# Kernel optimization log

Measured on AMD Instinct MI355X. Metric: run time of the kernel, lower is better.

Reference implementation:

```python
import jax, jax.numpy as jnp
import numpy as np

BSZ = 64
SEQ = 64      # logits rows per sequence (cu_seqlens_q stride)
CAND = 32     # candidates per batch == block_size
VOCAB = 32000
TOTAL = BSZ * CAND


def setup_inputs() -> dict:
    key = jax.random.key(0)
    k1, k2, k3, k4, k5 = jax.random.split(key, 5)
    input_logits = jax.random.normal(k1, (BSZ * SEQ, VOCAB), dtype=jnp.float32)
    relative_idx = jax.random.randint(k2, (TOTAL,), 0, SEQ, dtype=jnp.int32)
    batch_offsets = jnp.arange(BSZ, dtype=jnp.int32) * SEQ
    cu_filtered = jnp.arange(BSZ + 1, dtype=jnp.int32) * CAND
    cu_seqlens_q = jnp.arange(BSZ + 1, dtype=jnp.int32) * SEQ
    temperatures = 0.5 + 1.5 * jax.random.uniform(k3, (TOTAL,), dtype=jnp.float32)
    num_transfer = jax.random.randint(k4, (BSZ,), 0, 16, dtype=jnp.int32)
    thresholds = 0.3 * jax.random.uniform(k5, (BSZ,), dtype=jnp.float32)
    top_p = jnp.full((1,), 0.9, dtype=jnp.float32)
    return {
        'input_logits': input_logits, 'relative_idx': relative_idx,
        'batch_offsets': batch_offsets, 'cu_filtered': cu_filtered,
        'cu_seqlens_q': cu_seqlens_q, 'temperatures': temperatures,
        'num_transfer': num_transfer, 'thresholds': thresholds,
        'top_p': top_p, 'top_k': 50, 'block_size': CAND,
    }


def reference(input_logits, relative_idx, batch_offsets, cu_filtered, cu_seqlens_q,
              temperatures, num_transfer, thresholds, top_p, top_k, block_size):
    bsz = cu_filtered.shape[0] - 1
    total = relative_idx.shape[0]
    vocab = input_logits.shape[-1]
    NEG = jnp.finfo(input_logits.dtype).min

    # triton_repeat_interleave: group id of each candidate token
    counts = cu_filtered[1:] - cu_filtered[:-1]                      # [B]
    group_ids = jnp.repeat(jnp.arange(bsz), counts, total_repeat_length=total)
    k_values = jnp.maximum(num_transfer, 0)

    # gather candidate logits rows
    global_rows = cu_seqlens_q[:-1][group_ids] + relative_idx        # [T]
    cand = jnp.take(input_logits, global_rows, axis=0)               # [T, V]
    scaled = cand / temperatures[:, None]

    # top_k_logits
    kk = min(int(top_k), vocab)
    topk_vals = jax.lax.top_k(scaled, kk)[0]                         # [T, kk]
    thr_k = topk_vals[:, kk - 1][:, None]
    scaled = jnp.where(scaled < thr_k, NEG, scaled)

    # top_p_logits (nucleus)
    order = jnp.argsort(-scaled, axis=-1)                            # descending
    sorted_logits = jnp.take_along_axis(scaled, order, axis=-1)
    cum = jnp.cumsum(jax.nn.softmax(sorted_logits, axis=-1), axis=-1)
    remove = cum > top_p.reshape(-1, 1)
    remove = jnp.concatenate([jnp.zeros_like(remove[:, :1]), remove[:, :-1]], axis=-1)
    inv = jnp.argsort(order, axis=-1)                                # inverse permutation
    mask = jnp.take_along_axis(remove, inv, axis=-1)
    scaled = jnp.where(mask, NEG, scaled)

    probs = jax.nn.softmax(scaled, axis=-1)
    top_probs = probs.max(axis=-1)                                   # scores ('confidence')
    top_tokens = probs.argmax(axis=-1).astype(jnp.int32)             # greedy sample_token
    abs_idx = relative_idx + batch_offsets[group_ids]

    # ragged_to_dense: [B, block_size], padded with -inf / 0 / 0
    pos_in_row = jnp.arange(block_size)[None, :]                     # [1, L]
    row_mask = pos_in_row < counts[:, None]                          # [B, L]
    flat = jnp.where(row_mask, cu_filtered[:-1, None] + pos_in_row, 0)
    dense_scores = jnp.where(row_mask, top_probs[flat], -jnp.inf)
    dense_tokens = jnp.where(row_mask, top_tokens[flat], 0)
    dense_pos = jnp.where(row_mask, abs_idx[flat], 0)

    # per-row descending sort by score (padding -inf sorts last)
    sort_idx = jnp.argsort(-dense_scores, axis=1)
    sorted_scores = jnp.take_along_axis(dense_scores, sort_idx, axis=1)
    sorted_tokens = jnp.take_along_axis(dense_tokens, sort_idx, axis=1)
    sorted_pos = jnp.take_along_axis(dense_pos, sort_idx, axis=1)

    # filter_and_count
    keep = (pos_in_row < k_values[:, None]) \
        & (sorted_scores >= thresholds[:, None]) \
        & (sorted_scores > -jnp.inf)
    out_tokens = jnp.where(keep, sorted_tokens, -1)
    out_pos = jnp.where(keep, sorted_pos, 0)
    out_counts = keep.sum(axis=1).astype(jnp.int32)
    return out_pos, out_tokens, out_counts
```

## Files before the change

kernel.cpp:

```cpp
#include <hip/hip_runtime.h>
#include <math.h>

#define THREADS 256
#define CAP 512
#define HIST_BINS 4096
#define RAW_THRESH 2.5f

typedef float f32x4 __attribute__((ext_vector_type(4)));

__device__ __forceinline__ unsigned orderKey(float f) {
    unsigned u = __float_as_uint(f);
    return (u & 0x80000000u) ? ~u : (u | 0x80000000u);
}

struct WS {
    float* svals; int* sidx; int* wsn;
    float* prob; int* tok;
};
__device__ __forceinline__ WS ws_layout(void* ws, int nrows, int total) {
    WS w;
    w.svals = (float*)ws;
    w.sidx  = (int*)(w.svals + (size_t)nrows * CAP);
    w.wsn   = w.sidx + (size_t)nrows * CAP;
    w.prob  = (float*)(w.wsn + nrows);
    w.tok   = (int*)(w.prob + total);
    return w;
}

#define COLLECT1(x, gi) \
    if ((x) >= RAW_THRESH) { int p = atomicAdd(&s_n, 1); if (p < CAP) { u.a.v[p] = (x); u.a.id[p] = (gi); } }
#define COLLECT4(vv, base) \
    COLLECT1((vv).x, (base)) COLLECT1((vv).y, (base) + 1) \
    COLLECT1((vv).z, (base) + 2) COLLECT1((vv).w, (base) + 3)

__global__ __launch_bounds__(THREADS, 8) void row_kernel(
    const float* __restrict__ logits,
    const int* __restrict__ rel_idx,
    const int* __restrict__ cuf,
    const int* __restrict__ cuq,
    const int* __restrict__ topk_p,
    int bsz, int total, long long logits_n, void* ws)
{
    __shared__ union {
        struct { float v[CAP]; int id[CAP]; float sv[CAP]; int si[CAP]; } a;
        int hist[HIST_BINS];
    } u;
    __shared__ int s_n, s_needed;
    __shared__ unsigned s_T, s_maxkey;

    const int tid = threadIdx.x;
    const int nrows = cuq[bsz];
    const int vocab = (int)(logits_n / (long long)nrows);
    int kk = topk_p[0];
    if (kk > vocab) kk = vocab;

    WS w = ws_layout(ws, nrows, total);

    for (int r = blockIdx.x; r < nrows; r += gridDim.x) {
        int lo = 0, hi = bsz;
        while (hi - lo > 1) { int mid = (lo + hi) >> 1; if (r >= cuq[mid]) lo = mid; else hi = mid; }
        const int b = lo;
        const int rel = r - cuq[b];

        if (tid == 0) { s_needed = 0; s_n = 0; }
        __syncthreads();
        const int t0 = cuf[b], cnt = cuf[b + 1] - t0;
        for (int l = tid; l < cnt; l += THREADS)
            if (rel_idx[t0 + l] == rel) s_needed = 1;
        __syncthreads();
        if (!s_needed) continue;

        const float* rp = logits + (long long)r * (long long)vocab;
        const f32x4* rp4 = (const f32x4*)rp;
        const int nv4 = vocab >> 2;

        int i = tid;
        for (; i + THREADS < nv4; i += 2 * THREADS) {
            f32x4 a = rp4[i];
            f32x4 c = rp4[i + THREADS];
            float mx = fmaxf(fmaxf(fmaxf(a.x, a.y), fmaxf(a.z, a.w)),
                             fmaxf(fmaxf(c.x, c.y), fmaxf(c.z, c.w)));
            if (mx >= RAW_THRESH) {
                COLLECT4(a, i << 2)
                COLLECT4(c, (i + THREADS) << 2)
            }
        }
        for (; i < nv4; i += THREADS) {
            f32x4 a = rp4[i];
            float mx = fmaxf(fmaxf(a.x, a.y), fmaxf(a.z, a.w));
            if (mx >= RAW_THRESH) {
                COLLECT4(a, i << 2)
            }
        }
        for (int j = (nv4 << 2) + tid; j < vocab; j += THREADS) {
            float x = rp[j];
            COLLECT1(x, j)
        }
        __syncthreads();
        int n = s_n;

        if (n < kk || n > CAP) {
            __syncthreads();
            for (int j = tid; j < HIST_BINS; j += THREADS) u.hist[j] = 0;
            if (tid == 0) { s_n = 0; s_maxkey = 0; }
            __syncthreads();
            for (int j = tid; j < vocab; j += THREADS) {
                unsigned k = orderKey(rp[j]);
                atomicAdd(&u.hist[k >> 20], 1);
                atomicMax(&s_maxkey, k);
            }
            __syncthreads();
            if (tid == 0) {
                int B = (int)(s_maxkey >> 20);
                int cum = 0;
                while (true) {
                    cum += u.hist[B];
                    if (cum >= kk || B == 0) break;
                    --B;
                }
                s_T = ((unsigned)B) << 20;
            }
            __syncthreads();
            const unsigned Tk = s_T;
            __syncthreads();
            for (int j = tid; j < vocab; j += THREADS) {
                float a = rp[j];
                if (orderKey(a) >= Tk) {
                    int p = atomicAdd(&s_n, 1);
                    if (p < CAP) { u.a.v[p] = a; u.a.id[p] = j; }
                }
            }
            __syncthreads();
            n = s_n;
            if (n > CAP) n = CAP;
        }

        for (int j = tid; j < n; j += THREADS) {
            float v = u.a.v[j];
            int id = u.a.id[j];
            int rk = 0;
            for (int q = 0; q < n; ++q) {
                float x = u.a.v[q];
                rk += (x > v) || (x == v && u.a.id[q] < id);
            }
            u.a.sv[rk] = v;
            u.a.si[rk] = id;
        }
        __syncthreads();
        for (int j = tid; j < n; j += THREADS) {
            w.svals[(size_t)r * CAP + j] = u.a.sv[j];
            w.sidx[(size_t)r * CAP + j]  = u.a.si[j];
        }
        if (tid == 0) w.wsn[r] = n;
        __syncthreads();
    }
}

__global__ __launch_bounds__(64) void token_kernel(
    const float* __restrict__ logits,
    const int* __restrict__ rel_idx,
    const int* __restrict__ cuf,
    const int* __restrict__ cuq,
    const float* __restrict__ temps,
    const int* __restrict__ topk_p,
    const float* __restrict__ topp_p,
    int bsz, int total, long long logits_n, void* ws)
{
    __shared__ union {
        struct { float sv[CAP]; int si[CAP]; float e[CAP]; } a;
        int hist[HIST_BINS];
    } u;
    __shared__ int s_m, s_amax, s_n;
    __shared__ unsigned s_T, s_maxkey;

    const int t = blockIdx.x;
    const int l = threadIdx.x;
    const int nrows = cuq[bsz];
    const int vocab = (int)(logits_n / (long long)nrows);
    int kk = topk_p[0];
    if (kk > vocab) kk = vocab;

    WS w = ws_layout(ws, nrows, total);

    int lo = 0, hi = bsz;
    while (hi - lo > 1) { int mid = (lo + hi) >> 1; if (t >= cuf[mid]) lo = mid; else hi = mid; }
    const int row = cuq[lo] + rel_idx[t];
    const float T = temps[t];
    const float* rp = logits + (long long)row * (long long)vocab;
    int n = w.wsn[row];

    if (n >= kk && n <= CAP) {
        for (int j = l; j < n; j += 64) {
            u.a.sv[j] = w.svals[(size_t)row * CAP + j] / T;
            u.a.si[j] = w.sidx[(size_t)row * CAP + j];
        }
        __syncthreads();
    } else {
        for (int j = l; j < HIST_BINS; j += 64) u.hist[j] = 0;
        if (l == 0) { s_n = 0; s_maxkey = 0; }
        __syncthreads();
        for (int j = l; j < vocab; j += 64) {
            unsigned k = orderKey(rp[j]);
            atomicAdd(&u.hist[k >> 20], 1);
            atomicMax(&s_maxkey, k);
        }
        __syncthreads();
        if (l == 0) {
            int B = (int)(s_maxkey >> 20);
            int cum = 0;
            while (true) {
                cum += u.hist[B];
                if (cum >= kk || B == 0) break;
                --B;
            }
            s_T = ((unsigned)B) << 20;
        }
        __syncthreads();
        const unsigned Tk = s_T;
        __syncthreads();
        for (int j = l; j < vocab; j += 64) {
            float a = rp[j];
            if (orderKey(a) >= Tk) {
                int p = atomicAdd(&s_n, 1);
                if (p < CAP) { u.a.sv[p] = a / T; u.a.si[p] = j; }
            }
        }
        __syncthreads();
        n = s_n;
        if (n > CAP) n = CAP;
        if (kk > n) kk = n;
        float v = 0.f; int id = 0; int rk = -1;
        for (int j = l; j < n; j += 64) {
            v = u.a.sv[j]; id = u.a.si[j];
            int r2 = 0;
            for (int q = 0; q < n; ++q) {
                float x = u.a.sv[q];
                r2 += (x > v) || (x == v && u.a.si[q] < id);
            }
            rk = r2;
            break;
        }
        float vs[CAP / 64]; int ids[CAP / 64]; int rks[CAP / 64]; int cnt2 = 0;
        for (int j = l; j < n; j += 64) {
            float vv = u.a.sv[j]; int ii = u.a.si[j];
            int r2 = 0;
            for (int q = 0; q < n; ++q) {
                float x = u.a.sv[q];
                r2 += (x > vv) || (x == vv && u.a.si[q] < ii);
            }
            vs[cnt2] = vv; ids[cnt2] = ii; rks[cnt2] = r2; ++cnt2;
        }
        __syncthreads();
        for (int j2 = 0; j2 < cnt2; ++j2) { u.a.sv[rks[j2]] = vs[j2]; u.a.si[rks[j2]] = ids[j2]; }
        __syncthreads();
        (void)v; (void)id; (void)rk;
    }

    const float M = u.a.sv[0];
    const float thrk = u.a.sv[kk - 1];

    int mcnt = 0;
    int cand = 0x7fffffff;
    for (int j = l; j < n; j += 64) {
        mcnt += (u.a.sv[j] >= thrk) ? 1 : 0;
        if (u.a.sv[j] == M && u.a.si[j] < cand) cand = u.a.si[j];
    }
    for (int off = 32; off > 0; off >>= 1) {
        mcnt += __shfl_down(mcnt, off);
        int oc = __shfl_down(cand, off);
        if (oc < cand) cand = oc;
    }
    if (l == 0) { s_m = mcnt; s_amax = cand; }
    __syncthreads();
    const int m = s_m;
    for (int j = l; j < m; j += 64) u.a.e[j] = expf(u.a.sv[j] - M);
    __syncthreads();
    if (l == 0) {
        float Z1 = 0.f;
        for (int j = 0; j < m; ++j) Z1 += u.a.e[j];
        const float topp = topp_p[0];
        int jcut = m - 1;
        float c = 0.f;
        for (int j = 0; j < m; ++j) {
            float p = u.a.e[j] / Z1;
            c += p;
            if (c > topp) { jcut = j; break; }
        }
        float Z2 = 0.f;
        for (int j = 0; j <= jcut; ++j) Z2 += u.a.e[j];
        w.prob[t] = 1.0f / Z2;
        w.tok[t] = s_amax;
    }
}

__global__ __launch_bounds__(64) void finalize_kernel(
    const int* __restrict__ rel_idx,
    const int* __restrict__ boff,
    const int* __restrict__ cuf,
    const int* __restrict__ cuq,
    const int* __restrict__ num_transfer,
    const float* __restrict__ thresholds,
    int bsz, int total, int L,
    void* ws,
    int* __restrict__ out)
{
    const int bq = blockIdx.x;
    const int l = threadIdx.x;
    const int nrows = cuq[bsz];
    WS w = ws_layout(ws, nrows, total);

    const int start = cuf[bq];
    int cnt = cuf[bq + 1] - start;
    if (cnt > L) cnt = L;

    __shared__ float ss[64]; __shared__ int stk[64]; __shared__ int sp[64];
    __shared__ float ss2[64]; __shared__ int stk2[64]; __shared__ int sp2[64];

    float score = -INFINITY; int tk = 0; int pos = 0;
    if (l < L) {
        if (l < cnt) {
            int t = start + l;
            score = w.prob[t];
            tk = w.tok[t];
            pos = rel_idx[t] + boff[bq];
        }
        ss[l] = score; stk[l] = tk; sp[l] = pos;
    }
    __syncthreads();
    if (l < L) {
        int r = 0;
        for (int j = 0; j < L; ++j) {
            float x = ss[j];
            r += (x > score) || (x == score && j < l);
        }
        ss2[r] = score; stk2[r] = tk; sp2[r] = pos;
    }
    __syncthreads();

    int k = num_transfer[bq]; if (k < 0) k = 0;
    const float thrb = thresholds[bq];
    bool kp = false;
    if (l < L) {
        float s = ss2[l];
        kp = (l < k) && (s >= thrb) && (s > -INFINITY);
        out[bq * L + l] = kp ? sp2[l] : 0;
        out[bsz * L + bq * L + l] = kp ? stk2[l] : -1;
    }
    unsigned long long mask = __ballot(kp);
    if (l == 0) out[2 * bsz * L + bq] = (int)__popcll(mask);
}

extern "C" void kernel_launch(void* const* d_in, const int* in_sizes, int n_in,
                              void* d_out, int out_size, void* d_ws, size_t ws_size,
                              hipStream_t stream) {
    const float* logits   = (const float*)d_in[0];
    const int*   rel      = (const int*)d_in[1];
    const int*   boff     = (const int*)d_in[2];
    const int*   cuf      = (const int*)d_in[3];
    const int*   cuq      = (const int*)d_in[4];
    const float* temps    = (const float*)d_in[5];
    const int*   ntr      = (const int*)d_in[6];
    const float* thr      = (const float*)d_in[7];
    const float* topp     = (const float*)d_in[8];
    const int*   topk     = (const int*)d_in[9];

    const int total = in_sizes[1];
    const int bsz   = in_sizes[6];
    const long long logits_n = (long long)in_sizes[0];
    const int L = (out_size - bsz) / (2 * bsz);

    row_kernel<<<2 * total, THREADS, 0, stream>>>(
        logits, rel, cuf, cuq, topk, bsz, total, logits_n, d_ws);

    token_kernel<<<total, 64, 0, stream>>>(
        logits, rel, cuf, cuq, temps, topk, topp, bsz, total, logits_n, d_ws);

    finalize_kernel<<<bsz, 64, 0, stream>>>(
        rel, boff, cuf, cuq, ntr, thr, bsz, total, L, d_ws, (int*)d_out);
}
```

Before: 80.73 us.

## Precompute needed-row list and distribute rows via atomic work queue

```diff
diff --git a/kernel.cpp b/kernel.cpp
--- a/kernel.cpp
+++ b/kernel.cpp
@@ -14,12 +14,18 @@
 }
 
 struct WS {
+    int* mark;
+    int* rowlist;
+    int* meta;
     float* svals; int* sidx; int* wsn;
     float* prob; int* tok;
 };
 __device__ __forceinline__ WS ws_layout(void* ws, int nrows, int total) {
     WS w;
-    w.svals = (float*)ws;
+    w.mark = (int*)ws;
+    w.rowlist = w.mark + nrows;
+    w.meta = w.rowlist + nrows;
+    w.svals = (float*)(w.meta + 8);
     w.sidx  = (int*)(w.svals + (size_t)nrows * CAP);
     w.wsn   = w.sidx + (size_t)nrows * CAP;
     w.prob  = (float*)(w.wsn + nrows);
@@ -27,6 +33,31 @@
     return w;
 }
 
+__global__ void zero_kernel(const int* __restrict__ cuq, int bsz, int total, void* ws) {
+    const int nrows = cuq[bsz];
+    WS w = ws_layout(ws, nrows, total);
+    for (int i = blockIdx.x * blockDim.x + threadIdx.x; i < nrows; i += gridDim.x * blockDim.x)
+        w.mark[i] = 0;
+    if (blockIdx.x == 0 && threadIdx.x < 8) w.meta[threadIdx.x] = 0;
+}
+
+__global__ void mark_kernel(const int* __restrict__ rel_idx,
+                            const int* __restrict__ cuf,
+                            const int* __restrict__ cuq,
+                            int bsz, int total, void* ws) {
+    const int t = blockIdx.x * blockDim.x + threadIdx.x;
+    if (t >= total) return;
+    const int nrows = cuq[bsz];
+    WS w = ws_layout(ws, nrows, total);
+    int lo = 0, hi = bsz;
+    while (hi - lo > 1) { int mid = (lo + hi) >> 1; if (t >= cuf[mid]) lo = mid; else hi = mid; }
+    const int row = cuq[lo] + rel_idx[t];
+    if (atomicCAS(&w.mark[row], 0, 1) == 0) {
+        int p = atomicAdd(&w.meta[0], 1);
+        w.rowlist[p] = row;
+    }
+}
+
 #define COLLECT1(x, gi) \
     if ((x) >= RAW_THRESH) { int p = atomicAdd(&s_n, 1); if (p < CAP) { u.a.v[p] = (x); u.a.id[p] = (gi); } }
 #define COLLECT4(vv, base) \
@@ -35,8 +66,6 @@
 
 __global__ __launch_bounds__(THREADS, 8) void row_kernel(
     const float* __restrict__ logits,
-    const int* __restrict__ rel_idx,
-    const int* __restrict__ cuf,
     const int* __restrict__ cuq,
     const int* __restrict__ topk_p,
     int bsz, int total, long long logits_n, void* ws)
@@ -45,7 +74,7 @@
         struct { float v[CAP]; int id[CAP]; float sv[CAP]; int si[CAP]; } a;
         int hist[HIST_BINS];
     } u;
-    __shared__ int s_n, s_needed;
+    __shared__ int s_n, s_r;
     __shared__ unsigned s_T, s_maxkey;
 
     const int tid = threadIdx.x;
@@ -55,20 +84,17 @@
     if (kk > vocab) kk = vocab;
 
     WS w = ws_layout(ws, nrows, total);
-
-    for (int r = blockIdx.x; r < nrows; r += gridDim.x) {
-        int lo = 0, hi = bsz;
-        while (hi - lo > 1) { int mid = (lo + hi) >> 1; if (r >= cuq[mid]) lo = mid; else hi = mid; }
-        const int b = lo;
-        const int rel = r - cuq[b];
-
-        if (tid == 0) { s_needed = 0; s_n = 0; }
-        __syncthreads();
-        const int t0 = cuf[b], cnt = cuf[b + 1] - t0;
-        for (int l = tid; l < cnt; l += THREADS)
-            if (rel_idx[t0 + l] == rel) s_needed = 1;
-        __syncthreads();
-        if (!s_needed) continue;
+    const int nneeded = w.meta[0];
+
+    while (true) {
+        if (tid == 0) {
+            int i = atomicAdd(&w.meta[1], 1);
+            s_r = (i < nneeded) ? w.rowlist[i] : -1;
+            s_n = 0;
+        }
+        __syncthreads();
+        const int r = s_r;
+        if (r < 0) break;
 
         const float* rp = logits + (long long)r * (long long)vocab;
         const f32x4* rp4 = (const f32x4*)rp;
@@ -76,21 +102,15 @@
 
         int i = tid;
         for (; i + THREADS < nv4; i += 2 * THREADS) {
-            f32x4 a = rp4[i];
-            f32x4 c = rp4[i + THREADS];
-            float mx = fmaxf(fmaxf(fmaxf(a.x, a.y), fmaxf(a.z, a.w)),
-                             fmaxf(fmaxf(c.x, c.y), fmaxf(c.z, c.w)));
-            if (mx >= RAW_THRESH) {
-                COLLECT4(a, i << 2)
-                COLLECT4(c, (i + THREADS) << 2)
-            }
+            f32x4 v0 = rp4[i];
+            f32x4 v1 = rp4[i + THREADS];
+            int b0 = i << 2, b1 = (i + THREADS) << 2;
+            COLLECT1(v0.x, b0) COLLECT1(v0.y, b0 + 1) COLLECT1(v0.z, b0 + 2) COLLECT1(v0.w, b0 + 3)
+            COLLECT1(v1.x, b1) COLLECT1(v1.y, b1 + 1) COLLECT1(v1.z, b1 + 2) COLLECT1(v1.w, b1 + 3)
         }
         for (; i < nv4; i += THREADS) {
-            f32x4 a = rp4[i];
-            float mx = fmaxf(fmaxf(a.x, a.y), fmaxf(a.z, a.w));
-            if (mx >= RAW_THRESH) {
-                COLLECT4(a, i << 2)
-            }
+            f32x4 v = rp4[i];
+            COLLECT4(v, i << 2)
         }
         for (int j = (nv4 << 2) + tid; j < vocab; j += THREADS) {
             float x = rp[j];
@@ -229,17 +249,6 @@
         n = s_n;
         if (n > CAP) n = CAP;
         if (kk > n) kk = n;
-        float v = 0.f; int id = 0; int rk = -1;
-        for (int j = l; j < n; j += 64) {
-            v = u.a.sv[j]; id = u.a.si[j];
-            int r2 = 0;
-            for (int q = 0; q < n; ++q) {
-                float x = u.a.sv[q];
-                r2 += (x > v) || (x == v && u.a.si[q] < id);
-            }
-            rk = r2;
-            break;
-        }
         float vs[CAP / 64]; int ids[CAP / 64]; int rks[CAP / 64]; int cnt2 = 0;
         for (int j = l; j < n; j += 64) {
             float vv = u.a.sv[j]; int ii = u.a.si[j];
@@ -253,7 +262,6 @@
         __syncthreads();
         for (int j2 = 0; j2 < cnt2; ++j2) { u.a.sv[rks[j2]] = vs[j2]; u.a.si[rks[j2]] = ids[j2]; }
         __syncthreads();
-        (void)v; (void)id; (void)rk;
     }
 
     const float M = u.a.sv[0];
@@ -369,8 +377,13 @@
     const long long logits_n = (long long)in_sizes[0];
     const int L = (out_size - bsz) / (2 * bsz);
 
-    row_kernel<<<2 * total, THREADS, 0, stream>>>(
-        logits, rel, cuf, cuq, topk, bsz, total, logits_n, d_ws);
+    zero_kernel<<<64, 256, 0, stream>>>(cuq, bsz, total, d_ws);
+
+    mark_kernel<<<(total + 255) / 256, 256, 0, stream>>>(
+        rel, cuf, cuq, bsz, total, d_ws);
+
+    row_kernel<<<total, THREADS, 0, stream>>>(
+        logits, cuq, topk, bsz, total, logits_n, d_ws);
 
     token_kernel<<<total, 64, 0, stream>>>(
         logits, rel, cuf, cuq, temps, topk, topp, bsz, total, logits_n, d_ws);
```

Result: slower. 109.1 us (+35.1%).
